# Optimization experiments

Measured on AMD Instinct MI355X. Metric: run time of the kernel, lower is better.

Reference implementation:

```python
import jax, jax.numpy as jnp
import numpy as np

N_HEADS = 16
D_MODEL = 512
HEAD_DIM = D_MODEL // N_HEADS
SCALE = 1.0 / (HEAD_DIM ** 0.5)
R = 4  # LSREF radius -> window = step = 2*r = 8


def _layernorm(x, g, b, eps=1e-5):
    m = x.mean(axis=-1, keepdims=True)
    v = x.var(axis=-1, keepdims=True)
    return (x - m) / jnp.sqrt(v + eps) * g + b


def _mha(q_in, k_in, v_in, wq, bq, wk, bk, wv, bv, wo, bo):
    # Informer FullAttention(mask_flag=False), AttentionLayer(mix=False), eval mode (no dropout)
    B, L, _ = q_in.shape
    S = k_in.shape[1]
    q = (q_in @ wq.T + bq).reshape(B, L, N_HEADS, HEAD_DIM)
    k = (k_in @ wk.T + bk).reshape(B, S, N_HEADS, HEAD_DIM)
    v = (v_in @ wv.T + bv).reshape(B, S, N_HEADS, HEAD_DIM)
    scores = jnp.einsum('blhe,bshe->bhls', q, k) * SCALE
    A = jax.nn.softmax(scores, axis=-1)
    out = jnp.einsum('bhls,bshd->blhd', A, v).reshape(B, L, D_MODEL)
    return out @ wo.T + bo


def setup_inputs() -> dict:
    key = jax.random.key(0)
    ks = jax.random.split(key, 32)
    B, L, C, GL, DFF = 4, 1024, 512, 4096, 2048

    def w(k, shape, s=0.02):
        return (jax.random.normal(k, shape, jnp.float32) * s).astype(jnp.float32)

    inp = {
        'x': jax.random.normal(ks[0], (B, L, C), jnp.float32),
        'global_feat': jax.random.normal(ks[1], (B, C, GL), jnp.float32),
        'conv_w': w(ks[2], (C, C)), 'conv_b': jnp.zeros((C,), jnp.float32),
        'sa_wq': w(ks[3], (C, C)), 'sa_bq': jnp.zeros((C,), jnp.float32),
        'sa_wk': w(ks[4], (C, C)), 'sa_bk': jnp.zeros((C,), jnp.float32),
        'sa_wv': w(ks[5], (C, C)), 'sa_bv': jnp.zeros((C,), jnp.float32),
        'sa_wo': w(ks[6], (C, C)), 'sa_bo': jnp.zeros((C,), jnp.float32),
        'ca_wq': w(ks[7], (C, C)), 'ca_bq': jnp.zeros((C,), jnp.float32),
        'ca_wk': w(ks[8], (C, C)), 'ca_bk': jnp.zeros((C,), jnp.float32),
        'ca_wv': w(ks[9], (C, C)), 'ca_bv': jnp.zeros((C,), jnp.float32),
        'ca_wo': w(ks[10], (C, C)), 'ca_bo': jnp.zeros((C,), jnp.float32),
        'ffn_w1': w(ks[11], (DFF, C)), 'ffn_b1': jnp.zeros((DFF,), jnp.float32),
        'ffn_w2': w(ks[12], (C, DFF)), 'ffn_b2': jnp.zeros((C,), jnp.float32),
        'n1_g': jnp.ones((C,), jnp.float32), 'n1_b': jnp.zeros((C,), jnp.float32),
        'n2_g': jnp.ones((C,), jnp.float32), 'n2_b': jnp.zeros((C,), jnp.float32),
        'n3_g': jnp.ones((C,), jnp.float32), 'n3_b': jnp.zeros((C,), jnp.float32),
    }
    return inp


def reference(x, global_feat, conv_w, conv_b,
              sa_wq, sa_bq, sa_wk, sa_bk, sa_wv, sa_bv, sa_wo, sa_bo,
              ca_wq, ca_bq, ca_wk, ca_bk, ca_wv, ca_bv, ca_wo, ca_bo,
              ffn_w1, ffn_b1, ffn_w2, ffn_b2,
              n1_g, n1_b, n2_g, n2_b, n3_g, n3_b):
    # --- sliding_window_gaussian: non-overlapping windows (step == window == 2r) ---
    B, C, GL = global_feat.shape
    win_sz = 2 * R
    nw = (GL - win_sz) // win_sz + 1
    win = global_feat[:, :, :nw * win_sz].reshape(B, C, nw, win_sz)
    # torch.norm over a keepdim=1 axis is just |max - min|
    res = jnp.abs(win.max(axis=-1) - win.min(axis=-1)) + 1e-6  # [B, C, nw]
    # conv1d kernel size 1 == channelwise linear, then relu
    res = jax.nn.relu(jnp.einsum('oc,bcn->bon', conv_w, res) + conv_b[None, :, None])
    cross = res  # [B, 512, nw=512] consumed as [B, S, d_model]

    # --- CrossPyramidFusion: one Informer-style layer (self-attn, cross-attn, conv FFN) ---
    h = x + _mha(x, x, x, sa_wq, sa_bq, sa_wk, sa_bk, sa_wv, sa_bv, sa_wo, sa_bo)
    h = _layernorm(h, n1_g, n1_b)
    h = h + _mha(h, cross, cross, ca_wq, ca_bq, ca_wk, ca_bk, ca_wv, ca_bv, ca_wo, ca_bo)
    h = _layernorm(h, n2_g, n2_b)
    y = jax.nn.gelu(h @ ffn_w1.T + ffn_b1, approximate=False)
    y = y @ ffn_w2.T + ffn_b2
    out = _layernorm(h + y, n3_g, n3_b)
    return out.transpose(0, 2, 1)  # [B, 512, L]
```

## Files before the change

kernel.cpp:

```cpp
#include <hip/hip_runtime.h>
#include <hip/hip_bf16.h>
#include <math.h>

#define SCALE_ATTN 0.17677669529663687f
#define SCALE_Q 0.25504522f

typedef unsigned short u16;
typedef unsigned int u32;
typedef __attribute__((ext_vector_type(8))) short bshort8;
typedef __attribute__((ext_vector_type(4))) short sshort4;
typedef __attribute__((ext_vector_type(4))) float f32x4;
typedef __attribute__((ext_vector_type(4))) u32 u32x4;

__device__ inline u16 f2b(float f) {
    union { float f; uint32_t u; } c;
    c.f = f;
    uint32_t u = c.u;
    return (u16)((u + 0x7fffu + ((u >> 16) & 1u)) >> 16);
}

__device__ __forceinline__ u32 cvtpk(float a, float b) {
    u32 r;
    asm("v_cvt_pk_bf16_f32 %0, %1, %2" : "=v"(r) : "v"(a), "v"(b));
    return r;
}

__device__ __forceinline__ float exp2c(float s) {
    float c = fminf(s, 100.f);
    float r;
    asm("v_exp_f32 %0, %1" : "=v"(r) : "v"(c));
    return r;
}

__device__ inline void gload_lds16(const void* g, void* lds) {
    __builtin_amdgcn_global_load_lds(
        (const __attribute__((address_space(1))) void*)g,
        (__attribute__((address_space(3))) void*)lds, 16, 0, 0);
}

struct WSrc { const float* p[12]; };
__global__ __launch_bounds__(256) void wconv_kernel(WSrc s, u16* __restrict__ dst) {
    long e = ((long)blockIdx.x * 256 + threadIdx.x) * 4;
    if (e >= 6553600) return;
    int w; long base;
    if (e < 2359296)      { w = (int)(e >> 18); base = (long)w << 18; }
    else if (e < 3407872) { w = 9;  base = 2359296; }
    else if (e < 4456448) { w = 10; base = 3407872; }
    else                  { w = 11; base = 4456448; }
    float4 v = *(const float4*)(s.p[w] + (e - base));
    dst[e + 0] = f2b(v.x); dst[e + 1] = f2b(v.y);
    dst[e + 2] = f2b(v.z); dst[e + 3] = f2b(v.w);
}

__global__ __launch_bounds__(256) void win_kernel(const float* __restrict__ G,
                                                  u16* __restrict__ Rt, int total) {
    int i = blockIdx.x * 256 + threadIdx.x;
    if (i >= total) return;
    const float4* p = reinterpret_cast<const float4*>(G) + (size_t)i * 2;
    float4 a = p[0], b = p[1];
    float mx = fmaxf(fmaxf(fmaxf(a.x, a.y), fmaxf(a.z, a.w)),
                     fmaxf(fmaxf(b.x, b.y), fmaxf(b.z, b.w)));
    float mn = fminf(fminf(fminf(a.x, a.y), fminf(a.z, a.w)),
                     fminf(fminf(b.x, b.y), fminf(b.z, b.w)));
    int b_ = i >> 18, c = (i >> 9) & 511, n = i & 511;
    Rt[((long)(b_ * 512 + n) << 9) + c] = f2b(fabsf(mx - mn) + 1e-6f);
}

template <int BIASMODE, int ACT, bool RESID, int OUTMODE>
__global__ __launch_bounds__(256) void bgemm_kernel(
    const u16* __restrict__ A, const u16* __restrict__ Bt,
    const float* __restrict__ bias, const float* __restrict__ Rres,
    void* __restrict__ Cout, int M, int N, int K,
    long sA, long sB, long sC,
    u16* __restrict__ D1, u16* __restrict__ D2,
    const float* __restrict__ bias1, const float* __restrict__ bias2, int lbits) {
    A  += (long)blockIdx.z * sA;
    Bt += (long)blockIdx.z * sB;
    __shared__ u16 As[64 * 64];
    __shared__ u16 Bs[64 * 64];
    int tid = threadIdx.x;
    int lane = tid & 63, wv = tid >> 6;
    int wr = wv >> 1, wc = wv & 1;
    int m0 = blockIdx.x * 64, n0 = blockIdx.y * 64;
    f32x4 acc[2][2] = {};
    int srow = lane >> 3;
    int sbo = ((lane & 7) << 4) ^ (srow << 4);
    int selem = sbo >> 1;
    for (int k0 = 0; k0 < K; k0 += 64) {
        #pragma unroll
        for (int i = 0; i < 2; i++) {
            int r = i * 32 + wv * 8 + srow;
            gload_lds16(A + (long)(m0 + r) * K + k0 + selem,
                        (char*)As + (i * 32 + wv * 8) * 128);
            gload_lds16(Bt + (long)(n0 + r) * K + k0 + selem,
                        (char*)Bs + (i * 32 + wv * 8) * 128);
        }
        __syncthreads();
        #pragma unroll
        for (int ks = 0; ks < 2; ks++) {
            bshort8 af[2], bf[2];
            int kbo = ks * 64 + ((lane >> 4) << 4);
            #pragma unroll
            for (int f = 0; f < 2; f++) {
                int arow = wr * 32 + f * 16 + (lane & 15);
                af[f] = *(const bshort8*)((const char*)As + arow * 128 +
                                          (kbo ^ ((arow & 7) << 4)));
                int brow = wc * 32 + f * 16 + (lane & 15);
                bf[f] = *(const bshort8*)((const char*)Bs + brow * 128 +
                                          (kbo ^ ((brow & 7) << 4)));
            }
            #pragma unroll
            for (int fi = 0; fi < 2; fi++)
                #pragma unroll
                for (int fj = 0; fj < 2; fj++)
                    acc[fi][fj] = __builtin_amdgcn_mfma_f32_16x16x32_bf16(
                        af[fi], bf[fj], acc[fi][fj], 0, 0, 0);
        }
        __syncthreads();
    }
    #pragma unroll
    for (int fi = 0; fi < 2; fi++)
        #pragma unroll
        for (int fj = 0; fj < 2; fj++)
            #pragma unroll
            for (int r = 0; r < 4; r++) {
                int row = m0 + wr * 32 + fi * 16 + ((lane >> 4) << 2) + r;
                int col = n0 + wc * 32 + fj * 16 + (lane & 15);
                float v = acc[fi][fj][r];
                if (OUTMODE == 3) {
                    int grp = col >> 9, c = col & 511;
                    float bb = (grp == 0) ? bias[c] : (grp == 1) ? bias1[c] : bias2[c];
                    float vv = v + bb;
                    if (grp == 0)
                        ((u16*)Cout)[(long)row * 512 + c] = f2b(vv * SCALE_Q);
                    else if (grp == 1)
                        D1[(long)row * 512 + c] = f2b(vv);
                    else
                        D2[((long)((row >> 10) * 512 + c) << 10) + (row & 1023)] = f2b(vv);
                } else if (OUTMODE == 4) {
                    int grp = col >> 9, c = col & 511;
                    float vv = v + ((grp == 0) ? bias[c] : bias1[c]);
                    if (grp == 0)
                        ((u16*)Cout)[(long)row * 512 + c] = f2b(vv);
                    else
                        D2[((long)((row >> 9) * 512 + c) << 9) + (row & 511)] = f2b(vv);
                } else {
                    if (BIASMODE == 1) v += bias[col];
                    if (BIASMODE == 2) v += bias[row];
                    if (ACT == 1) v = fmaxf(v, 0.f);
                    if (ACT == 2) v = 0.5f * v * (1.f + erff(v * 0.70710678118654752f));
                    if (ACT == 3) v *= SCALE_Q;
                    if (RESID) v += Rres[(long)row * N + col];
                    if (OUTMODE == 2) {
                        int rl = row & ((1 << lbits) - 1);
                        long off = ((long)(row >> lbits) * N + col) << lbits;
                        ((u16*)Cout)[off + rl] = f2b(v);
                    } else {
                        long off = (long)blockIdx.z * sC + (long)row * N + col;
                        if (OUTMODE == 1) ((u16*)Cout)[off] = f2b(v);
                        else              ((float*)Cout)[off] = v;
                    }
                }
            }
}

__global__ __launch_bounds__(256) void attn_mfma_kernel(
    const u16* __restrict__ Q, const u16* __restrict__ K,
    const u16* __restrict__ Vt, u16* __restrict__ O, int L, int S) {
    __shared__ __align__(16) u16 Ks[2][2048];
    __shared__ __align__(16) u16 Vs[2][2048];
    int bh = blockIdx.x;
    int b = bh >> 4, h = bh & 15;
    int tid = threadIdx.x;
    int lane = tid & 63, wv = tid >> 6;
    int q0 = blockIdx.y * 64 + wv * 16;
    int qr = lane & 15, g = lane >> 4, g8 = g * 8;
    int kperm = 8 * (qr >> 2) + (qr & 3);

    const u16* Kb = K + (long)b * S * 512 + h * 32;
    const u16* Vb = Vt + ((long)b * 512 + h * 32) * S;
    bshort8 qf = *(const bshort8*)(Q + ((long)(b * L + q0 + qr)) * 512 + h * 32 + g8);

    const u16* ksrc = Kb + (long)(wv * 16 + (lane >> 2)) * 512 + ((lane & 3) << 3);
    const u16* vsrc = Vb + (long)(wv * 8 + (lane >> 3)) * S + ((lane & 7) << 3);

    f32x4 acc0 = {}, acc1 = {};
    float lsum = 0.f;

    int nt = S >> 6;
    gload_lds16(ksrc, (char*)Ks[0] + wv * 1024);
    gload_lds16(vsrc, (char*)Vs[0] + wv * 1024);
    int cur = 0;
    for (int t = 0; t < nt; ++t) {
        if (t + 1 < nt) {
            int s0 = (t + 1) << 6;
            gload_lds16(ksrc + (long)s0 * 512, (char*)Ks[cur ^ 1] + wv * 1024);
            gload_lds16(vsrc + s0, (char*)Vs[cur ^ 1] + wv * 1024);
            asm volatile("s_waitcnt vmcnt(2)\ns_barrier" ::: "memory");
        } else {
            asm volatile("s_waitcnt vmcnt(0)\ns_barrier" ::: "memory");
        }
        const u16* Kt = Ks[cur];
        const u16* Vl = Vs[cur];
        bshort8 a0 = *(const bshort8*)(Kt + kperm * 32 + g8);
        bshort8 a1 = *(const bshort8*)(Kt + (kperm + 4) * 32 + g8);
        bshort8 a2 = *(const bshort8*)(Kt + (kperm + 32) * 32 + g8);
        bshort8 a3 = *(const bshort8*)(Kt + (kperm + 36) * 32 + g8);
        bshort8 v00 = *(const bshort8*)(Vl + qr * 64 + g8);
        bshort8 v01 = *(const bshort8*)(Vl + qr * 64 + 32 + g8);
        bshort8 v10 = *(const bshort8*)(Vl + (16 + qr) * 64 + g8);
        bshort8 v11 = *(const bshort8*)(Vl + (16 + qr) * 64 + 32 + g8);
        f32x4 z = {0.f, 0.f, 0.f, 0.f};
        f32x4 st0 = __builtin_amdgcn_mfma_f32_16x16x32_bf16(a0, qf, z, 0, 0, 0);
        f32x4 st1 = __builtin_amdgcn_mfma_f32_16x16x32_bf16(a1, qf, z, 0, 0, 0);
        f32x4 st2 = __builtin_amdgcn_mfma_f32_16x16x32_bf16(a2, qf, z, 0, 0, 0);
        f32x4 st3 = __builtin_amdgcn_mfma_f32_16x16x32_bf16(a3, qf, z, 0, 0, 0);
        float p0[4], p1[4], p2[4], p3[4];
        #pragma unroll
        for (int r = 0; r < 4; r++) {
            p0[r] = exp2c(st0[r]);
            p1[r] = exp2c(st1[r]);
            p2[r] = exp2c(st2[r]);
            p3[r] = exp2c(st3[r]);
        }
        float ps = ((p0[0] + p0[1]) + (p0[2] + p0[3])) + ((p1[0] + p1[1]) + (p1[2] + p1[3])) +
                   ((p2[0] + p2[1]) + (p2[2] + p2[3])) + ((p3[0] + p3[1]) + (p3[2] + p3[3]));
        lsum += ps;
        u32x4 P0 = { cvtpk(p0[0], p0[1]), cvtpk(p0[2], p0[3]),
                     cvtpk(p1[0], p1[1]), cvtpk(p1[2], p1[3]) };
        u32x4 P1 = { cvtpk(p2[0], p2[1]), cvtpk(p2[2], p2[3]),
                     cvtpk(p3[0], p3[1]), cvtpk(p3[2], p3[3]) };
        bshort8 pf0 = *(bshort8*)&P0;
        bshort8 pf1 = *(bshort8*)&P1;
        acc0 = __builtin_amdgcn_mfma_f32_16x16x32_bf16(v00, pf0, acc0, 0, 0, 0);
        acc0 = __builtin_amdgcn_mfma_f32_16x16x32_bf16(v01, pf1, acc0, 0, 0, 0);
        acc1 = __builtin_amdgcn_mfma_f32_16x16x32_bf16(v10, pf0, acc1, 0, 0, 0);
        acc1 = __builtin_amdgcn_mfma_f32_16x16x32_bf16(v11, pf1, acc1, 0, 0, 0);
        asm volatile("s_barrier" ::: "memory");
        cur ^= 1;
    }

    lsum += __shfl_xor(lsum, 16);
    lsum += __shfl_xor(lsum, 32);
    float inv = 1.f / lsum;
    u16* op = O + ((long)(b * L + q0 + qr)) * 512 + h * 32 + g * 4;
    sshort4 o0, o1;
    #pragma unroll
    for (int r = 0; r < 4; r++) {
        o0[r] = (short)f2b(acc0[r] * inv);
        o1[r] = (short)f2b(acc1[r] * inv);
    }
    *(sshort4*)op = o0;
    *(sshort4*)(op + 16) = o1;
}

template <bool TRANS, bool DUAL>
__global__ __launch_bounds__(256) void ln_kernel(const float* __restrict__ X,
                                                 const float* __restrict__ g,
                                                 const float* __restrict__ bt,
                                                 float* __restrict__ Y,
                                                 u16* __restrict__ Yb) {
    int row = blockIdx.x;
    const float* xr = X + (long)row * 512;
    int t = threadIdx.x;
    float x0 = xr[t], x1 = xr[t + 256];
    float s = x0 + x1, ss = x0 * x0 + x1 * x1;
    #pragma unroll
    for (int off = 32; off > 0; off >>= 1) {
        s += __shfl_down(s, off);
        ss += __shfl_down(ss, off);
    }
    __shared__ float sred[4], ssred[4];
    int wid = t >> 6;
    if ((t & 63) == 0) { sred[wid] = s; ssred[wid] = ss; }
    __syncthreads();
    float ts = sred[0] + sred[1] + sred[2] + sred[3];
    float tss = ssred[0] + ssred[1] + ssred[2] + ssred[3];
    float mean = ts * (1.f / 512.f);
    float var = tss * (1.f / 512.f) - mean * mean;
    float rstd = rsqrtf(var + 1e-5f);
    float y0 = (x0 - mean) * rstd * g[t] + bt[t];
    float y1 = (x1 - mean) * rstd * g[t + 256] + bt[t + 256];
    if (TRANS) {
        int b = row >> 10, l = row & 1023;
        Y[((long)b * 512 + t) * 1024 + l] = y0;
        Y[((long)b * 512 + t + 256) * 1024 + l] = y1;
    } else {
        Y[(long)row * 512 + t] = y0;
        Y[(long)row * 512 + t + 256] = y1;
    }
    if (DUAL) {
        Yb[(long)row * 512 + t] = f2b(y0);
        Yb[(long)row * 512 + t + 256] = f2b(y1);
    }
}

extern "C" void kernel_launch(void* const* d_in, const int* in_sizes, int n_in,
                              void* d_out, int out_size, void* d_ws, size_t ws_size,
                              hipStream_t stream) {
    const float* x      = (const float*)d_in[0];
    const float* gfeat  = (const float*)d_in[1];
    const float* conv_w = (const float*)d_in[2];
    const float* conv_b = (const float*)d_in[3];
    const float* sa_wq = (const float*)d_in[4];
    const float* sa_bq = (const float*)d_in[5];
    const float* sa_wk = (const float*)d_in[6];
    const float* sa_bk = (const float*)d_in[7];
    const float* sa_wv = (const float*)d_in[8];
    const float* sa_bv = (const float*)d_in[9];
    const float* sa_wo = (const float*)d_in[10];
    const float* sa_bo = (const float*)d_in[11];
    const float* ca_wq = (const float*)d_in[12];
    const float* ca_bq = (const float*)d_in[13];
    const float* ca_wk = (const float*)d_in[14];
    const float* ca_bk = (const float*)d_in[15];
    const float* ca_wv = (const float*)d_in[16];
    const float* ca_bv = (const float*)d_in[17];
    const float* ca_wo = (const float*)d_in[18];
    const float* ca_bo = (const float*)d_in[19];
    const float* ffn_w1 = (const float*)d_in[20];
    const float* ffn_b1 = (const float*)d_in[21];
    const float* ffn_w2 = (const float*)d_in[22];
    const float* ffn_b2 = (const float*)d_in[23];
    const float* n1_g = (const float*)d_in[24];
    const float* n1_b = (const float*)d_in[25];
    const float* n2_g = (const float*)d_in[26];
    const float* n2_b = (const float*)d_in[27];
    const float* n3_g = (const float*)d_in[28];
    const float* n3_b = (const float*)d_in[29];
    (void)ws_size; (void)n_in; (void)in_sizes; (void)out_size;

    const long M_ = 1048576;
    float* W0 = (float*)d_ws;
    float* h   = W0;
    float* hn  = W0 + 2 * M_;
    u16* U = (u16*)(W0 + 4 * M_);
    u16* qb     = U;
    u16* kb     = U + 2 * M_;
    u16* vtb    = U + 4 * M_;
    u16* k2b    = U + 6 * M_;
    u16* v2tb   = U + 7 * M_;
    u16* attb   = U + 8 * M_;
    u16* hnb    = U + 10 * M_;
    u16* midb   = U + 12 * M_;
    u16* wsb    = U + 20 * M_;
    u16* res_tb = U + 27 * M_;
    u16* crossb = U + 28 * M_;

    const u16* conv_wb = wsb;
    const u16* sa_wqb = wsb + 262144;
    const u16* sa_wob = wsb + 1048576;
    const u16* ca_wqb = wsb + 1310720;
    const u16* ca_wkb = wsb + 1572864;
    const u16* ca_wob = wsb + 2097152;
    const u16* ffn1b = wsb + 2359296, *ffn2b = wsb + 3407872;
    const u16* xb = wsb + 4456448;

    WSrc ws;
    ws.p[0] = conv_w; ws.p[1] = sa_wq; ws.p[2] = sa_wk; ws.p[3] = sa_wv;
    ws.p[4] = sa_wo; ws.p[5] = ca_wq; ws.p[6] = ca_wk; ws.p[7] = ca_wv;
    ws.p[8] = ca_wo; ws.p[9] = ffn_w1; ws.p[10] = ffn_w2; ws.p[11] = x;
    wconv_kernel<<<6400, 256, 0, stream>>>(ws, wsb);

    win_kernel<<<4096, 256, 0, stream>>>(gfeat, res_tb, 4 * 512 * 512);

    bgemm_kernel<2, 1, false, 1><<<dim3(8, 8, 4), 256, 0, stream>>>(
        conv_wb, res_tb, conv_b, nullptr, crossb, 512, 512, 512, 0, 262144, 262144,
        nullptr, nullptr, nullptr, nullptr, 0);

    bgemm_kernel<1, 0, false, 3><<<dim3(64, 24), 256, 0, stream>>>(
        xb, sa_wqb, sa_bq, nullptr, qb, 4096, 1536, 512, 0, 0, 0,
        kb, vtb, sa_bk, sa_bv, 10);

    attn_mfma_kernel<<<dim3(64, 16), 256, 0, stream>>>(qb, kb, vtb, attb, 1024, 1024);

    bgemm_kernel<1, 0, true, 0><<<dim3(64, 8), 256, 0, stream>>>(
        attb, sa_wob, sa_bo, x, h, 4096, 512, 512, 0, 0, 0,
        nullptr, nullptr, nullptr, nullptr, 0);

    ln_kernel<false, true><<<4096, 256, 0, stream>>>(h, n1_g, n1_b, hn, hnb);

    bgemm_kernel<1, 3, false, 1><<<dim3(64, 8), 256, 0, stream>>>(
        hnb, ca_wqb, ca_bq, nullptr, qb, 4096, 512, 512, 0, 0, 0,
        nullptr, nullptr, nullptr, nullptr, 0);
    bgemm_kernel<1, 0, false, 4><<<dim3(32, 16), 256, 0, stream>>>(
        crossb, ca_wkb, ca_bk, nullptr, k2b, 2048, 1024, 512, 0, 0, 0,
        nullptr, v2tb, ca_bv, nullptr, 9);

    attn_mfma_kernel<<<dim3(64, 16), 256, 0, stream>>>(qb, k2b, v2tb, attb, 1024, 512);

    bgemm_kernel<1, 0, true, 0><<<dim3(64, 8), 256, 0, stream>>>(
        attb, ca_wob, ca_bo, hn, h, 4096, 512, 512, 0, 0, 0,
        nullptr, nullptr, nullptr, nullptr, 0);

    ln_kernel<false, true><<<4096, 256, 0, stream>>>(h, n2_g, n2_b, hn, hnb);

    bgemm_kernel<1, 2, false, 1><<<dim3(64, 32), 256, 0, stream>>>(
        hnb, ffn1b, ffn_b1, nullptr, midb, 4096, 2048, 512, 0, 0, 0,
        nullptr, nullptr, nullptr, nullptr, 0);

    bgemm_kernel<1, 0, true, 0><<<dim3(64, 8), 256, 0, stream>>>(
        midb, ffn2b, ffn_b2, hn, h, 4096, 512, 2048, 0, 0, 0,
        nullptr, nullptr, nullptr, nullptr, 0);

    ln_kernel<true, false><<<4096, 256, 0, stream>>>(h, n3_g, n3_b, (float*)d_out, nullptr);
}
```

Before: 193.2 us.

## Enlarge GEMM tiles to 128x128 and split attention over key halves

The GEMM kernel moves from 64x64 to 128x128 output tiles, giving each wave a 4x4 set of MFMA fragments so each staged input is reused more. Attention now runs 512-thread blocks where half the waves load K and half load V, with XOR-swizzled LDS layouts to cut bank conflicts. The key dimension is split into two halves across blockIdx.z, writing unnormalized fp32 partial outputs and row sums, which a new combine kernel adds and normalizes. In exchange the change adds fp32 partial-buffer traffic and an extra launch, and the GEMM grids shrink to few blocks (for example 128 for the N=512 GEMMs), which may underfill the GPU's compute units.

```diff
diff --git a/kernel.cpp b/kernel.cpp
--- a/kernel.cpp
+++ b/kernel.cpp
@@ -2,7 +2,6 @@
 #include <hip/hip_bf16.h>
 #include <math.h>
 
-#define SCALE_ATTN 0.17677669529663687f
 #define SCALE_Q 0.25504522f
 
 typedef unsigned short u16;
@@ -73,59 +72,58 @@
     void* __restrict__ Cout, int M, int N, int K,
     long sA, long sB, long sC,
     u16* __restrict__ D1, u16* __restrict__ D2,
-    const float* __restrict__ bias1, const float* __restrict__ bias2, int lbits) {
+    const float* __restrict__ bias1, const float* __restrict__ bias2) {
     A  += (long)blockIdx.z * sA;
     Bt += (long)blockIdx.z * sB;
-    __shared__ u16 As[64 * 64];
-    __shared__ u16 Bs[64 * 64];
+    __shared__ u16 As[128 * 64];
+    __shared__ u16 Bs[128 * 64];
     int tid = threadIdx.x;
     int lane = tid & 63, wv = tid >> 6;
     int wr = wv >> 1, wc = wv & 1;
-    int m0 = blockIdx.x * 64, n0 = blockIdx.y * 64;
-    f32x4 acc[2][2] = {};
+    int m0 = blockIdx.x * 128, n0 = blockIdx.y * 128;
+    f32x4 acc[4][4] = {};
     int srow = lane >> 3;
-    int sbo = ((lane & 7) << 4) ^ (srow << 4);
-    int selem = sbo >> 1;
+    int selem = (((lane & 7) ^ srow) << 3);
     for (int k0 = 0; k0 < K; k0 += 64) {
         #pragma unroll
-        for (int i = 0; i < 2; i++) {
-            int r = i * 32 + wv * 8 + srow;
+        for (int p = 0; p < 4; p++) {
+            int r = p * 32 + wv * 8 + srow;
             gload_lds16(A + (long)(m0 + r) * K + k0 + selem,
-                        (char*)As + (i * 32 + wv * 8) * 128);
+                        (char*)As + (p * 32 + wv * 8) * 128);
             gload_lds16(Bt + (long)(n0 + r) * K + k0 + selem,
-                        (char*)Bs + (i * 32 + wv * 8) * 128);
+                        (char*)Bs + (p * 32 + wv * 8) * 128);
         }
         __syncthreads();
         #pragma unroll
         for (int ks = 0; ks < 2; ks++) {
-            bshort8 af[2], bf[2];
+            bshort8 af[4], bf[4];
             int kbo = ks * 64 + ((lane >> 4) << 4);
             #pragma unroll
-            for (int f = 0; f < 2; f++) {
-                int arow = wr * 32 + f * 16 + (lane & 15);
+            for (int f = 0; f < 4; f++) {
+                int arow = wr * 64 + f * 16 + (lane & 15);
                 af[f] = *(const bshort8*)((const char*)As + arow * 128 +
                                           (kbo ^ ((arow & 7) << 4)));
-                int brow = wc * 32 + f * 16 + (lane & 15);
+                int brow = wc * 64 + f * 16 + (lane & 15);
                 bf[f] = *(const bshort8*)((const char*)Bs + brow * 128 +
                                           (kbo ^ ((brow & 7) << 4)));
             }
             #pragma unroll
-            for (int fi = 0; fi < 2; fi++)
+            for (int fi = 0; fi < 4; fi++)
                 #pragma unroll
-                for (int fj = 0; fj < 2; fj++)
+                for (int fj = 0; fj < 4; fj++)
                     acc[fi][fj] = __builtin_amdgcn_mfma_f32_16x16x32_bf16(
                         af[fi], bf[fj], acc[fi][fj], 0, 0, 0);
         }
         __syncthreads();
     }
     #pragma unroll
-    for (int fi = 0; fi < 2; fi++)
+    for (int fi = 0; fi < 4; fi++)
         #pragma unroll
-        for (int fj = 0; fj < 2; fj++)
+        for (int fj = 0; fj < 4; fj++)
             #pragma unroll
             for (int r = 0; r < 4; r++) {
-                int row = m0 + wr * 32 + fi * 16 + ((lane >> 4) << 2) + r;
-                int col = n0 + wc * 32 + fj * 16 + (lane & 15);
+                int row = m0 + wr * 64 + fi * 16 + ((lane >> 4) << 2) + r;
+                int col = n0 + wc * 64 + fj * 16 + (lane & 15);
                 float v = acc[fi][fj][r];
                 if (OUTMODE == 3) {
                     int grp = col >> 9, c = col & 511;
@@ -151,70 +149,80 @@
                     if (ACT == 2) v = 0.5f * v * (1.f + erff(v * 0.70710678118654752f));
                     if (ACT == 3) v *= SCALE_Q;
                     if (RESID) v += Rres[(long)row * N + col];
-                    if (OUTMODE == 2) {
-                        int rl = row & ((1 << lbits) - 1);
-                        long off = ((long)(row >> lbits) * N + col) << lbits;
-                        ((u16*)Cout)[off + rl] = f2b(v);
-                    } else {
-                        long off = (long)blockIdx.z * sC + (long)row * N + col;
-                        if (OUTMODE == 1) ((u16*)Cout)[off] = f2b(v);
-                        else              ((float*)Cout)[off] = v;
-                    }
+                    long off = (long)blockIdx.z * sC + (long)row * N + col;
+                    if (OUTMODE == 1) ((u16*)Cout)[off] = f2b(v);
+                    else              ((float*)Cout)[off] = v;
                 }
             }
 }
 
-__global__ __launch_bounds__(256) void attn_mfma_kernel(
+__global__ __launch_bounds__(512) void attn_mfma_kernel(
     const u16* __restrict__ Q, const u16* __restrict__ K,
-    const u16* __restrict__ Vt, u16* __restrict__ O, int L, int S) {
+    const u16* __restrict__ Vt, float* __restrict__ Pacc0,
+    float* __restrict__ Pacc1, float* __restrict__ Pml, int L, int S) {
     __shared__ __align__(16) u16 Ks[2][2048];
     __shared__ __align__(16) u16 Vs[2][2048];
     int bh = blockIdx.x;
     int b = bh >> 4, h = bh & 15;
+    int z = blockIdx.z;
     int tid = threadIdx.x;
     int lane = tid & 63, wv = tid >> 6;
-    int q0 = blockIdx.y * 64 + wv * 16;
+    int q0 = blockIdx.y * 128 + wv * 16;
     int qr = lane & 15, g = lane >> 4, g8 = g * 8;
     int kperm = 8 * (qr >> 2) + (qr & 3);
+    int sbeg = z * (S >> 1);
+    int nt = S >> 7;
 
     const u16* Kb = K + (long)b * S * 512 + h * 32;
     const u16* Vb = Vt + ((long)b * 512 + h * 32) * S;
     bshort8 qf = *(const bshort8*)(Q + ((long)(b * L + q0 + qr)) * 512 + h * 32 + g8);
 
-    const u16* ksrc = Kb + (long)(wv * 16 + (lane >> 2)) * 512 + ((lane & 3) << 3);
-    const u16* vsrc = Vb + (long)(wv * 8 + (lane >> 3)) * S + ((lane & 7) << 3);
+    const u16* src;
+    long step;
+    char *d0, *d1;
+    if (wv < 4) {
+        int rk = wv * 16 + (lane >> 2);
+        int sc = (lane & 3) ^ ((lane >> 3) & 3);
+        src = Kb + (long)(sbeg + rk) * 512 + sc * 8;
+        step = (long)64 * 512;
+        d0 = (char*)Ks[0] + wv * 1024;
+        d1 = (char*)Ks[1] + wv * 1024;
+    } else {
+        int rv = (wv - 4) * 8 + (lane >> 3);
+        int sc = (lane & 7) ^ (lane >> 3);
+        src = Vb + (long)rv * S + sbeg + sc * 8;
+        step = 64;
+        d0 = (char*)Vs[0] + (wv - 4) * 1024;
+        d1 = (char*)Vs[1] + (wv - 4) * 1024;
+    }
 
     f32x4 acc0 = {}, acc1 = {};
     float lsum = 0.f;
 
-    int nt = S >> 6;
-    gload_lds16(ksrc, (char*)Ks[0] + wv * 1024);
-    gload_lds16(vsrc, (char*)Vs[0] + wv * 1024);
+    gload_lds16(src, d0);
     int cur = 0;
     for (int t = 0; t < nt; ++t) {
         if (t + 1 < nt) {
-            int s0 = (t + 1) << 6;
-            gload_lds16(ksrc + (long)s0 * 512, (char*)Ks[cur ^ 1] + wv * 1024);
-            gload_lds16(vsrc + s0, (char*)Vs[cur ^ 1] + wv * 1024);
-            asm volatile("s_waitcnt vmcnt(2)\ns_barrier" ::: "memory");
+            gload_lds16(src + (long)(t + 1) * step, cur ? d0 : d1);
+            asm volatile("s_waitcnt vmcnt(1)\ns_barrier" ::: "memory");
         } else {
             asm volatile("s_waitcnt vmcnt(0)\ns_barrier" ::: "memory");
         }
-        const u16* Kt = Ks[cur];
-        const u16* Vl = Vs[cur];
-        bshort8 a0 = *(const bshort8*)(Kt + kperm * 32 + g8);
-        bshort8 a1 = *(const bshort8*)(Kt + (kperm + 4) * 32 + g8);
-        bshort8 a2 = *(const bshort8*)(Kt + (kperm + 32) * 32 + g8);
-        bshort8 a3 = *(const bshort8*)(Kt + (kperm + 36) * 32 + g8);
-        bshort8 v00 = *(const bshort8*)(Vl + qr * 64 + g8);
-        bshort8 v01 = *(const bshort8*)(Vl + qr * 64 + 32 + g8);
-        bshort8 v10 = *(const bshort8*)(Vl + (16 + qr) * 64 + g8);
-        bshort8 v11 = *(const bshort8*)(Vl + (16 + qr) * 64 + 32 + g8);
-        f32x4 z = {0.f, 0.f, 0.f, 0.f};
-        f32x4 st0 = __builtin_amdgcn_mfma_f32_16x16x32_bf16(a0, qf, z, 0, 0, 0);
-        f32x4 st1 = __builtin_amdgcn_mfma_f32_16x16x32_bf16(a1, qf, z, 0, 0, 0);
-        f32x4 st2 = __builtin_amdgcn_mfma_f32_16x16x32_bf16(a2, qf, z, 0, 0, 0);
-        f32x4 st3 = __builtin_amdgcn_mfma_f32_16x16x32_bf16(a3, qf, z, 0, 0, 0);
+        const char* Kt = (const char*)Ks[cur];
+        const char* Vl = (const char*)Vs[cur];
+        bshort8 a0 = *(const bshort8*)(Kt + kperm * 64 + ((g ^ ((kperm >> 1) & 3)) << 4));
+        bshort8 a1 = *(const bshort8*)(Kt + (kperm + 4) * 64 + ((g ^ (((kperm + 4) >> 1) & 3)) << 4));
+        bshort8 a2 = *(const bshort8*)(Kt + (kperm + 32) * 64 + ((g ^ (((kperm + 32) >> 1) & 3)) << 4));
+        bshort8 a3 = *(const bshort8*)(Kt + (kperm + 36) * 64 + ((g ^ (((kperm + 36) >> 1) & 3)) << 4));
+        bshort8 v00 = *(const bshort8*)(Vl + qr * 128 + ((g ^ (qr & 7)) << 4));
+        bshort8 v01 = *(const bshort8*)(Vl + qr * 128 + (((g + 4) ^ (qr & 7)) << 4));
+        bshort8 v10 = *(const bshort8*)(Vl + (16 + qr) * 128 + ((g ^ (qr & 7)) << 4));
+        bshort8 v11 = *(const bshort8*)(Vl + (16 + qr) * 128 + (((g + 4) ^ (qr & 7)) << 4));
+        f32x4 zz = {0.f, 0.f, 0.f, 0.f};
+        f32x4 st0 = __builtin_amdgcn_mfma_f32_16x16x32_bf16(a0, qf, zz, 0, 0, 0);
+        f32x4 st1 = __builtin_amdgcn_mfma_f32_16x16x32_bf16(a1, qf, zz, 0, 0, 0);
+        f32x4 st2 = __builtin_amdgcn_mfma_f32_16x16x32_bf16(a2, qf, zz, 0, 0, 0);
+        f32x4 st3 = __builtin_amdgcn_mfma_f32_16x16x32_bf16(a3, qf, zz, 0, 0, 0);
         float p0[4], p1[4], p2[4], p3[4];
         #pragma unroll
         for (int r = 0; r < 4; r++) {
@@ -242,16 +250,37 @@
 
     lsum += __shfl_xor(lsum, 16);
     lsum += __shfl_xor(lsum, 32);
-    float inv = 1.f / lsum;
-    u16* op = O + ((long)(b * L + q0 + qr)) * 512 + h * 32 + g * 4;
+    float* PZ = z ? Pacc1 : Pacc0;
+    float* pa = PZ + (((long)b * L + q0 + qr) << 9) + h * 32 + g * 4;
+    *(f32x4*)pa = acc0;
+    *(f32x4*)(pa + 16) = acc1;
+    if (g == 0) Pml[(long)z * 65536 + (long)bh * L + q0 + qr] = lsum;
+}
+
+__global__ __launch_bounds__(256) void attn_combine_kernel(
+    const float* __restrict__ P0, const float* __restrict__ P1,
+    const float* __restrict__ Pml, u16* __restrict__ O) {
+    long e = ((long)blockIdx.x * 256 + threadIdx.x) * 8;
+    int q = (int)(e >> 9);
+    int c = (int)(e & 511);
+    int h = c >> 5;
+    int b = q >> 10, l = q & 1023;
+    int bh = b * 16 + h;
+    float l0 = Pml[bh * 1024 + l];
+    float l1 = Pml[65536 + bh * 1024 + l];
+    float inv = 1.f / (l0 + l1);
+    f32x4 x0 = *(const f32x4*)(P0 + e);
+    f32x4 x1 = *(const f32x4*)(P0 + e + 4);
+    f32x4 y0 = *(const f32x4*)(P1 + e);
+    f32x4 y1 = *(const f32x4*)(P1 + e + 4);
     sshort4 o0, o1;
     #pragma unroll
     for (int r = 0; r < 4; r++) {
-        o0[r] = (short)f2b(acc0[r] * inv);
-        o1[r] = (short)f2b(acc1[r] * inv);
-    }
-    *(sshort4*)op = o0;
-    *(sshort4*)(op + 16) = o1;
+        o0[r] = (short)f2b((x0[r] + y0[r]) * inv);
+        o1[r] = (short)f2b((x1[r] + y1[r]) * inv);
+    }
+    *(sshort4*)(O + e) = o0;
+    *(sshort4*)(O + e + 4) = o1;
 }
 
 template <bool TRANS, bool DUAL>
@@ -347,6 +376,13 @@
     u16* res_tb = U + 27 * M_;
     u16* crossb = U + 28 * M_;
 
+    float* sP0 = h;
+    float* sP1 = hn;
+    float* sPml = (float*)midb;
+    float* cP0 = (float*)(U + 2 * M_);
+    float* cP1 = (float*)(U + 12 * M_);
+    float* cPml = (float*)(U + 16 * M_);
+
     const u16* conv_wb = wsb;
     const u16* sa_wqb = wsb + 262144;
     const u16* sa_wob = wsb + 1048576;
@@ -364,44 +400,48 @@
 
     win_kernel<<<4096, 256, 0, stream>>>(gfeat, res_tb, 4 * 512 * 512);
 
-    bgemm_kernel<2, 1, false, 1><<<dim3(8, 8, 4), 256, 0, stream>>>(
+    bgemm_kernel<2, 1, false, 1><<<dim3(4, 4, 4), 256, 0, stream>>>(
         conv_wb, res_tb, conv_b, nullptr, crossb, 512, 512, 512, 0, 262144, 262144,
-        nullptr, nullptr, nullptr, nullptr, 0);
-
-    bgemm_kernel<1, 0, false, 3><<<dim3(64, 24), 256, 0, stream>>>(
+        nullptr, nullptr, nullptr, nullptr);
+
+    bgemm_kernel<1, 0, false, 3><<<dim3(32, 12), 256, 0, stream>>>(
         xb, sa_wqb, sa_bq, nullptr, qb, 4096, 1536, 512, 0, 0, 0,
-        kb, vtb, sa_bk, sa_bv, 10);
-
-    attn_mfma_kernel<<<dim3(64, 16), 256, 0, stream>>>(qb, kb, vtb, attb, 1024, 1024);
-
-    bgemm_kernel<1, 0, true, 0><<<dim3(64, 8), 256, 0, stream>>>(
+        kb, vtb, sa_bk, sa_bv);
+
+    attn_mfma_kernel<<<dim3(64, 8, 2), 512, 0, stream>>>(
+        qb, kb, vtb, sP0, sP1, sPml, 1024, 1024);
+    attn_combine_kernel<<<1024, 256, 0, stream>>>(sP0, sP1, sPml, attb);
+
+    bgemm_kernel<1, 0, true, 0><<<dim3(32, 4), 256, 0, stream>>>(
         attb, sa_wob, sa_bo, x, h, 4096, 512, 512, 0, 0, 0,
-        nullptr, nullptr, nullptr, nullptr, 0);
+        nullptr, nullptr, nullptr, nullptr);
 
     ln_kernel<false, true><<<4096, 256, 0, stream>>>(h, n1_g, n1_b, hn, hnb);
 
-    bgemm_kernel<1, 3, false, 1><<<dim3(64, 8), 256, 0, stream>>>(
+    bgemm_kernel<1, 3, false, 1><<<dim3(32, 4), 256, 0, stream>>>(
         hnb, ca_wqb, ca_bq, nullptr, qb, 4096, 512, 512, 0, 0, 0,
-        nullptr, nullptr, nullptr, nullptr, 0);
-    bgemm_kernel<1, 0, false, 4><<<dim3(32, 16), 256, 0, stream>>>(
+        nullptr, nullptr, nullptr, nullptr);
+    bgemm_kernel<1, 0, false, 4><<<dim3(16, 8), 256, 0, stream>>>(
         crossb, ca_wkb, ca_bk, nullptr, k2b, 2048, 1024, 512, 0, 0, 0,
-        nullptr, v2tb, ca_bv, nullptr, 9);
-
-    attn_mfma_kernel<<<dim3(64, 16), 256, 0, stream>>>(qb, k2b, v2tb, attb, 1024, 512);
-
-    bgemm_kernel<1, 0, true, 0><<<dim3(64, 8), 256, 0, stream>>>(
+        nullptr, v2tb, ca_bv, nullptr);
+
+    attn_mfma_kernel<<<dim3(64, 8, 2), 512, 0, stream>>>(
+        qb, k2b, v2tb, cP0, cP1, cPml, 1024, 512);
+    attn_combine_kernel<<<1024, 256, 0, stream>>>(cP0, cP1, cPml, attb);
+
+    bgemm_kernel<1, 0, true, 0><<<dim3(32, 4), 256, 0, stream>>>(
         attb, ca_wob, ca_bo, hn, h, 4096, 512, 512, 0, 0, 0,
-        nullptr, nullptr, nullptr, nullptr, 0);
+        nullptr, nullptr, nullptr, nullptr);
 
     ln_kernel<false, true><<<4096, 256, 0, stream>>>(h, n2_g, n2_b, hn, hnb);
 
-    bgemm_kernel<1, 2, false, 1><<<dim3(64, 32), 256, 0, stream>>>(
+    bgemm_kernel<1, 2, false, 1><<<dim3(32, 16), 256, 0, stream>>>(
         hnb, ffn1b, ffn_b1, nullptr, midb, 4096, 2048, 512, 0, 0, 0,
-        nullptr, nullptr, nullptr, nullptr, 0);
-
-    bgemm_kernel<1, 0, true, 0><<<dim3(64, 8), 256, 0, stream>>>(
+        nullptr, nullptr, nullptr, nullptr);
+
+    bgemm_kernel<1, 0, true, 0><<<dim3(32, 4), 256, 0, stream>>>(
         midb, ffn2b, ffn_b2, hn, h, 4096, 512, 2048, 0, 0, 0,
-        nullptr, nullptr, nullptr, nullptr, 0);
+        nullptr, nullptr, nullptr, nullptr);
 
     ln_kernel<true, false><<<4096, 256, 0, stream>>>(h, n3_g, n3_b, (float*)d_out, nullptr);
 }
```

New measurement: 248.5 us. 1.29x slower.
